# Kernel tuning notes

Measured on AMD Instinct MI355X. Metric: run time of the kernel, lower is better.

## Reference

```python
import jax, jax.numpy as jnp
import numpy as np

B, S, E = 2, 2048, 1024
H, D = 16, 64  # num_heads, head_size; H*D == E

def setup_inputs() -> dict:
    key = jax.random.key(0)
    k1, k2, k3 = jax.random.split(key, 3)
    x = jax.random.normal(k1, (B, S, E), dtype=jnp.float32)
    w_qkv = jax.random.normal(k2, (E, 3 * H * D), dtype=jnp.float32) / np.sqrt(E)
    b_qkv = jnp.zeros((3 * H * D,), dtype=jnp.float32)
    w_out = jax.random.normal(k3, (H * D, E), dtype=jnp.float32) / np.sqrt(H * D)
    b_out = jnp.zeros((E,), dtype=jnp.float32)
    return {"x": x, "w_qkv": w_qkv, "b_qkv": b_qkv, "w_out": w_out, "b_out": b_out}

def reference(x, w_qkv, b_qkv, w_out, b_out):
    b, s, e = x.shape
    qkv = x @ w_qkv + b_qkv                       # [b, s, 3*H*D]
    qkv = qkv.reshape(b, s, 3, H, D).transpose(2, 0, 3, 1, 4)  # [3, b, H, s, D]
    q, k, v = qkv[0], qkv[1], qkv[2]
    scores = jnp.einsum('bhqd,bhkd->bhqk', q, k) / jnp.sqrt(jnp.float32(D))
    mask = jnp.tril(jnp.ones((s, s), dtype=scores.dtype))
    scores = scores * mask - 1e10 * (1 - mask)
    attn = jax.nn.softmax(scores, axis=-1)
    out = jnp.einsum('bhqk,bhkd->bhqd', attn, v)  # [b, H, s, D]
    out = out.transpose(0, 2, 1, 3).reshape(b, s, H * D)
    return out @ w_out + b_out
```

## Files before the change

kernel.cpp:

```cpp
#include <hip/hip_runtime.h>

typedef unsigned short u16;
typedef __attribute__((ext_vector_type(8))) short bf16x8;
typedef __attribute__((ext_vector_type(4))) float f32x4;

#define S_LEN 2048
#define MTOT  4096
#define LOG2E_DIV8 0.1803368784f

__device__ inline u16 f2bf(float f) {
  union { float f; unsigned u; } x; x.f = f;
  unsigned r = x.u + 0x7fffu + ((x.u >> 16) & 1u);
  return (u16)(r >> 16);
}
__device__ inline float bf2f(u16 u) {
  union { unsigned u; float f; } x; x.u = ((unsigned)u) << 16;
  return x.f;
}

__device__ __forceinline__ unsigned cvtpk_bf16(float lo, float hi) {
  unsigned r;
  asm("v_cvt_pk_bf16_f32 %0, %1, %2" : "=v"(r) : "v"(lo), "v"(hi));
  return r;
}
__device__ __forceinline__ float fexp2(float x) {
  float r;
  asm("v_exp_f32 %0, %1" : "=v"(r) : "v"(x));
  return r;
}
__device__ __forceinline__ float frcp(float x) {
  float r;
  asm("v_rcp_f32 %0, %1" : "=v"(r) : "v"(x));
  return r;
}

#define SWAP32(a, b) asm("v_permlane32_swap_b32 %0, %1" : "+v"(a), "+v"(b))
#define SWAP16(a, b) asm("v_permlane16_swap_b32 %0, %1" : "+v"(a), "+v"(b))

__device__ __forceinline__ float sum_lg(float x) {
  float a = x, b = x;
  SWAP32(a, b);
  float s = a + b;
  float c = s, d = s;
  SWAP16(c, d);
  return c + d;
}

typedef __attribute__((address_space(1))) const unsigned int gu32;
typedef __attribute__((address_space(3))) unsigned int lu32;
__device__ __forceinline__ void gload_lds16(const void* g, void* l) {
  __builtin_amdgcn_global_load_lds((gu32*)g, (lu32*)l, 16, 0, 0);
}

#define MFMA16(a, b, c) __builtin_amdgcn_mfma_f32_16x16x32_bf16((a), (b), (c), 0, 0, 0)
#define BAR  __builtin_amdgcn_s_barrier()
#define VMC6 asm volatile("s_waitcnt vmcnt(6)" ::: "memory")
#define VMC0 asm volatile("s_waitcnt vmcnt(0)" ::: "memory")

__global__ __launch_bounds__(256) void prep(const float* __restrict__ x,
                                            const float* __restrict__ wqkv,
                                            const float* __restrict__ wout,
                                            u16* __restrict__ x_bf,
                                            u16* __restrict__ dqkv,
                                            u16* __restrict__ dwout) {
  __shared__ float tile[64][65];
  int bid = blockIdx.x;
  int t = threadIdx.x;
  if (bid < 4096) {
    int i = (bid * 256 + t) * 4;
    float4 v = *(const float4*)(x + i);
    ushort4 o;
    o.x = f2bf(v.x); o.y = f2bf(v.y); o.z = f2bf(v.z); o.w = f2bf(v.w);
    *(ushort4*)(x_bf + i) = o;
    return;
  }
  int idx = bid - 4096;
  int bx = idx & 63, by = idx >> 6;
  const float* src; u16* dst; int N, n0;
  if (bx < 48) { src = wqkv; dst = dqkv; N = 3072; n0 = bx * 64; }
  else         { src = wout; dst = dwout; N = 1024; n0 = (bx - 48) * 64; }
  int K = 1024, k0 = by * 64;
  for (int i = 0; i < 16; ++i) {
    int id2 = t + 256 * i;
    int r = id2 >> 6, c = id2 & 63;
    tile[r][c] = src[(size_t)(k0 + r) * N + n0 + c];
  }
  __syncthreads();
  for (int i = 0; i < 16; ++i) {
    int id2 = t + 256 * i;
    int r = id2 >> 6, c = id2 & 63;
    dst[(size_t)(n0 + r) * K + k0 + c] = f2bf(tile[c][r]);
  }
}

__global__ __launch_bounds__(512, 1) void gemm_qkv(const u16* __restrict__ A,
                                                   const u16* __restrict__ Bt,
                                                   const float* __restrict__ bias,
                                                   u16* __restrict__ qkv,
                                                   u16* __restrict__ Vt,
                                                   float qscale) {
  __shared__ __align__(16) u16 smem[65536];
  int t = threadIdx.x;
  int w = t >> 6, l = t & 63;
  int wr = w >> 2, wcn = w & 3;
  int lr = l & 15, lg = l >> 4;

  int bid = blockIdx.y * 12 + blockIdx.x;
  int orig = (bid & 7) * 24 + (bid >> 3);
  int bx = orig % 12, by = orig / 12;
  int m0 = by * 256, n0 = bx * 256;

  f32x4 acc[8][4];
#pragma unroll
  for (int i = 0; i < 8; ++i)
#pragma unroll
    for (int j = 0; j < 4; ++j)
      acc[i][j] = f32x4{0.f, 0.f, 0.f, 0.f};

  int cg = ((t & 7) ^ ((t >> 3) & 7)) * 8;
  const u16* gAh[2][2];
  const u16* gBh[2][2];
#pragma unroll
  for (int h = 0; h < 2; ++h)
#pragma unroll
    for (int j = 0; j < 2; ++j) {
      gAh[h][j] = A  + (size_t)(m0 + h * 128 + j * 64 + (t >> 3)) * 1024 + cg;
      gBh[h][j] = Bt + (size_t)(n0 + h * 128 + j * 64 + (t >> 3)) * 1024 + cg;
    }

#define STG_A(kt, h) {                                                  \
    u16* d_ = smem + (((kt) & 1) * 2 + (h)) * 8192 + t * 8;             \
    gload_lds16(gAh[h][0] + (size_t)(kt) * 64, d_);                     \
    gload_lds16(gAh[h][1] + (size_t)(kt) * 64, d_ + 4096);              }
#define STG_B(kt, h) {                                                  \
    u16* d_ = smem + 32768 + (((kt) & 1) * 2 + (h)) * 8192 + t * 8;     \
    gload_lds16(gBh[h][0] + (size_t)(kt) * 64, d_);                     \
    gload_lds16(gBh[h][1] + (size_t)(kt) * 64, d_ + 4096);              }

  int o0 = lr * 64 + ((lg ^ (lr & 7)) << 3);
  int o1 = lr * 64 + (((4 + lg) ^ (lr & 7)) << 3);
  const u16* bA[2] = { smem + wr * 8192, smem + (2 + wr) * 8192 };
  const u16* bB[2] = { smem + 32768 + (wcn >> 1) * 8192 + (wcn & 1) * 4096,
                       smem + 32768 + (2 + (wcn >> 1)) * 8192 + (wcn & 1) * 4096 };

  bf16x8 AF[4][2], Bf[4][2];
#define LDA(B_, OFF) { const u16* p_ = bA[B_] + (OFF);                  \
    _Pragma("unroll") for (int mi = 0; mi < 4; ++mi) {                  \
      AF[mi][0] = *(const bf16x8*)(p_ + mi * 1024 + o0);                \
      AF[mi][1] = *(const bf16x8*)(p_ + mi * 1024 + o1); } }
#define LDB(B_) { const u16* p_ = bB[B_];                               \
    _Pragma("unroll") for (int ni = 0; ni < 4; ++ni) {                  \
      Bf[ni][0] = *(const bf16x8*)(p_ + ni * 1024 + o0);                \
      Bf[ni][1] = *(const bf16x8*)(p_ + ni * 1024 + o1); } }
#define QUAD(MO, NO) {                                                  \
    __builtin_amdgcn_s_setprio(1);                                      \
    _Pragma("unroll") for (int mi = 0; mi < 4; ++mi)                    \
    _Pragma("unroll") for (int ni = 0; ni < 2; ++ni) {                  \
      acc[MO + mi][NO + ni] = MFMA16(AF[mi][0], Bf[NO + ni][0], acc[MO + mi][NO + ni]); \
      acc[MO + mi][NO + ni] = MFMA16(AF[mi][1], Bf[NO + ni][1], acc[MO + mi][NO + ni]); } \
    __builtin_amdgcn_s_setprio(0); }

  STG_B(0, 0); STG_B(0, 1); STG_A(0, 0); STG_A(0, 1);
  STG_B(1, 0); STG_B(1, 1); STG_A(1, 0);
  VMC6;
  BAR;

  for (int i = 0; i < 8; ++i) {
    bool s = (i < 7);
    int k0t = 2 * i, k1t = 2 * i + 1;
    LDA(0, 0); LDB(0);
    STG_A(k1t, 1);
    BAR; QUAD(0, 0); BAR;
    if (s) STG_B(k0t + 2, 0);
    BAR; QUAD(0, 2); BAR;
    LDA(0, 4096);
    if (s) STG_B(k0t + 2, 1);
    BAR; QUAD(4, 0); BAR;
    if (s) STG_A(k0t + 2, 0);
    if (i == 7) { VMC0; } else { VMC6; }
    BAR; QUAD(4, 2); BAR;
    LDA(1, 0); LDB(1);
    if (s) STG_A(k0t + 2, 1);
    BAR; QUAD(0, 0); BAR;
    if (s) STG_B(k1t + 2, 0);
    BAR; QUAD(0, 2); BAR;
    LDA(1, 4096);
    if (s) STG_B(k1t + 2, 1);
    BAR; QUAD(4, 0); BAR;
    if (s) STG_A(k1t + 2, 0);
    VMC6;
    BAR; QUAD(4, 2); BAR;
  }
#undef STG_A
#undef STG_B
#undef LDA
#undef LDB
#undef QUAD

  if (bx < 8) {
    float qs = (bx < 4) ? qscale : 1.0f;
#pragma unroll
    for (int mi = 0; mi < 8; ++mi)
#pragma unroll
      for (int ni = 0; ni < 4; ++ni)
#pragma unroll
        for (int rg = 0; rg < 4; ++rg) {
          int row = m0 + wr * 128 + mi * 16 + lg * 4 + rg;
          int col = n0 + wcn * 64 + ni * 16 + lr;
          qkv[(size_t)row * 3072 + col] = f2bf((acc[mi][ni][rg] + bias[col]) * qs);
        }
    return;
  }

  int b = by >> 3, sbase = (by & 7) * 256;
  u16* Vl = smem;
#pragma unroll 1
  for (int g = 0; g < 4; ++g) {
    __syncthreads();
    if (wcn == g) {
#pragma unroll
      for (int mi = 0; mi < 8; ++mi)
#pragma unroll
        for (int ni = 0; ni < 4; ++ni) {
          int d = ni * 16 + lr;
          int srow = wr * 128 + mi * 16 + lg * 4;
          int col = n0 + g * 64 + d;
          union { u16 u[4]; unsigned long long q; } pk;
#pragma unroll
          for (int rg = 0; rg < 4; ++rg)
            pk.u[rg] = f2bf(acc[mi][ni][rg] + bias[col]);
          *(unsigned long long*)&Vl[d * 272 + srow] = pk.q;
        }
    }
    __syncthreads();
    int hv = (bx - 8) * 4 + g;
    int d = t >> 3, sc = (t & 7) * 32;
    u16* dst = Vt + ((size_t)((b * 16 + hv) * 64 + d)) * 2048 + sbase + sc;
    const u16* src = Vl + d * 272 + sc;
#pragma unroll
    for (int j = 0; j < 4; ++j)
      *(uint4*)(dst + j * 8) = *(const uint4*)(src + j * 8);
  }
}

__global__ __launch_bounds__(256) void gemm_bt64(const u16* __restrict__ A,
                                                 const u16* __restrict__ Bt,
                                                 const float* __restrict__ bias,
                                                 float* __restrict__ C,
                                                 int N, int K) {
  __shared__ __align__(16) u16 smem[2][6144];
  int t = threadIdx.x;
  int w = t >> 6, l = t & 63;
  int lr = l & 15, lg = l >> 4;

  int nwg = gridDim.x * gridDim.y;
  int bid = blockIdx.y * gridDim.x + blockIdx.x;
  int orig = (bid & 7) * (nwg >> 3) + (bid >> 3);
  int bx = orig % gridDim.x, by = orig / gridDim.x;
  int m0 = by * 64, n0 = bx * 128;

  f32x4 acc[4][2];
#pragma unroll
  for (int i = 0; i < 4; ++i)
#pragma unroll
    for (int j = 0; j < 2; ++j)
      acc[i][j] = f32x4{0.f, 0.f, 0.f, 0.f};

  int ra = w * 16 + (l >> 2);
  int ca = (l & 3) ^ ((ra >> 1) & 3);
  int rb1 = ra + 64;
  int cb1 = (l & 3) ^ ((rb1 >> 1) & 3);
  const u16* gA  = A  + (size_t)(m0 + ra) * K + ca * 8;
  const u16* gB0 = Bt + (size_t)(n0 + ra) * K + ca * 8;
  const u16* gB1 = Bt + (size_t)(n0 + rb1) * K + cb1 * 8;
  int oA  = (w * 16) * 32;
  int oB0 = 2048 + (w * 16) * 32;
  int oB1 = 2048 + (64 + w * 16) * 32;

#define STAGE(K0, BUF) {                                   \
    gload_lds16(gA + (K0), &smem[BUF][oA]);                \
    gload_lds16(gB0 + (K0), &smem[BUF][oB0]);              \
    gload_lds16(gB1 + (K0), &smem[BUF][oB1]);              }

  STAGE(0, 0);
  __syncthreads();
  int cur = 0;
  for (int k0 = 0; k0 < K; k0 += 32) {
    if (k0 + 32 < K) STAGE(k0 + 32, cur ^ 1);
    const u16* As = smem[cur];
    const u16* Bs = smem[cur] + 2048;
    bf16x8 af[4], bfr[2];
#pragma unroll
    for (int mi = 0; mi < 4; ++mi) {
      int row = mi * 16 + lr;
      af[mi] = *(const bf16x8*)(As + row * 32 + ((lg ^ ((row >> 1) & 3)) << 3));
    }
#pragma unroll
    for (int ni = 0; ni < 2; ++ni) {
      int row = w * 32 + ni * 16 + lr;
      bfr[ni] = *(const bf16x8*)(Bs + row * 32 + ((lg ^ ((row >> 1) & 3)) << 3));
    }
    __builtin_amdgcn_s_setprio(1);
#pragma unroll
    for (int mi = 0; mi < 4; ++mi)
#pragma unroll
      for (int ni = 0; ni < 2; ++ni)
        acc[mi][ni] = MFMA16(af[mi], bfr[ni], acc[mi][ni]);
    __builtin_amdgcn_s_setprio(0);
    __syncthreads();
    cur ^= 1;
  }
#undef STAGE

#pragma unroll
  for (int mi = 0; mi < 4; ++mi)
#pragma unroll
    for (int ni = 0; ni < 2; ++ni)
#pragma unroll
      for (int rg = 0; rg < 4; ++rg) {
        int row = m0 + mi * 16 + lg * 4 + rg;
        int col = n0 + w * 32 + ni * 16 + lr;
        C[(size_t)row * N + col] = acc[mi][ni][rg] + bias[col];
      }
}

__device__ __forceinline__ void attn_tile(const u16* Ks, const u16* Vs,
                                          bf16x8 q0, bf16x8 q1, f32x4* o,
                                          float& l_run, bool diag,
                                          int w, int l, int lr, int lg) {
  f32x4 s[4];
  __builtin_amdgcn_s_setprio(1);
#pragma unroll
  for (int ct = 0; ct < 4; ++ct) {
    int row = ct * 16 + lr;
    bf16x8 kf0 = *(const bf16x8*)(Ks + ((row * 64 + lg * 8) ^ ((row & 7) << 3)));
    bf16x8 kf1 = *(const bf16x8*)(Ks + ((row * 64 + 32 + lg * 8) ^ ((row & 7) << 3)));
    f32x4 z = f32x4{0.f, 0.f, 0.f, 0.f};
    z = MFMA16(kf0, q0, z);
    z = MFMA16(kf1, q1, z);
    s[ct] = z;
  }
  __builtin_amdgcn_s_setprio(0);
  if (diag) {
    int qrel = w * 16 + lr;
#pragma unroll
    for (int ct = 0; ct < 4; ++ct)
#pragma unroll
      for (int rg = 0; rg < 4; ++rg)
        if ((ct * 16 + lg * 4 + rg) > qrel) s[ct][rg] = -1e30f;
  }
  float ps = 0.f;
#pragma unroll
  for (int ct = 0; ct < 4; ++ct)
#pragma unroll
    for (int rg = 0; rg < 4; ++rg) {
      float p = fexp2(s[ct][rg]);
      s[ct][rg] = p;
      ps += p;
    }
  l_run += sum_lg(ps);

  unsigned W00 = cvtpk_bf16(s[0][0], s[0][1]);
  unsigned W01 = cvtpk_bf16(s[0][2], s[0][3]);
  unsigned W10 = cvtpk_bf16(s[1][0], s[1][1]);
  unsigned W11 = cvtpk_bf16(s[1][2], s[1][3]);
  unsigned W20 = cvtpk_bf16(s[2][0], s[2][1]);
  unsigned W21 = cvtpk_bf16(s[2][2], s[2][3]);
  unsigned W30 = cvtpk_bf16(s[3][0], s[3][1]);
  unsigned W31 = cvtpk_bf16(s[3][2], s[3][3]);
  SWAP32(W00, W10); SWAP16(W00, W10);
  SWAP32(W01, W11); SWAP16(W01, W11);
  SWAP32(W20, W30); SWAP16(W20, W30);
  SWAP32(W21, W31); SWAP16(W21, W31);
  union { unsigned u[4]; bf16x8 v; } P0, P1;
  P0.u[0] = W00; P0.u[1] = W01; P0.u[2] = W10; P0.u[3] = W11;
  P1.u[0] = W20; P1.u[1] = W21; P1.u[2] = W30; P1.u[3] = W31;

  __builtin_amdgcn_s_setprio(1);
#pragma unroll
  for (int dt = 0; dt < 4; ++dt) {
    int row = dt * 16 + lr;
    bf16x8 vf0 = *(const bf16x8*)(Vs + ((row * 64 + lg * 8) ^ ((row & 7) << 3)));
    bf16x8 vf1 = *(const bf16x8*)(Vs + ((row * 64 + 32 + lg * 8) ^ ((row & 7) << 3)));
    o[dt] = MFMA16(P0.v, vf0, o[dt]);
    o[dt] = MFMA16(P1.v, vf1, o[dt]);
  }
  __builtin_amdgcn_s_setprio(0);
}

__global__ __launch_bounds__(256, 4) void attn_kernel(const u16* __restrict__ qkv,
                                                      const u16* __restrict__ Vt,
                                                      u16* __restrict__ po0,
                                                      u16* __restrict__ po1,
                                                      float* __restrict__ pl) {
  __shared__ __align__(16) u16 Ks[2][64 * 64];
  __shared__ __align__(16) u16 Vs[2][64 * 64];
  int bid = blockIdx.y * 32 + blockIdx.x;
  int orig = (bid & 7) * 128 + (bid >> 3);
  int half = orig & 1;
  int qtA = (orig >> 1) & 15;
  int bh = orig >> 5;
  int qtB = 31 - qtA;
  int m = (qtA >= 8) ? 8 : (15 - qtA);
  int kts = half ? m : 0;
  int kte = half ? (qtB + 1) : m;
  int b = bh >> 4, h = bh & 15;
  int t = threadIdx.x, w = t >> 6, l = t & 63;
  int lr = l & 15, lg = l >> 4;

  const u16* qbase = qkv + (size_t)b * S_LEN * 3072 + h * 64;
  int qrA = qtA * 64 + w * 16 + lr;
  int qrB = qtB * 64 + w * 16 + lr;
  bf16x8 qA0 = *(const bf16x8*)(qbase + (size_t)qrA * 3072 + lg * 8);
  bf16x8 qA1 = *(const bf16x8*)(qbase + (size_t)qrA * 3072 + 32 + lg * 8);
  bf16x8 qB0 = *(const bf16x8*)(qbase + (size_t)qrB * 3072 + lg * 8);
  bf16x8 qB1 = *(const bf16x8*)(qbase + (size_t)qrB * 3072 + 32 + lg * 8);

  f32x4 oA[4], oB[4];
#pragma unroll
  for (int i = 0; i < 4; ++i) { oA[i] = f32x4{0.f,0.f,0.f,0.f}; oB[i] = f32x4{0.f,0.f,0.f,0.f}; }
  float lA = 0.f, lB = 0.f;

  int r0s = t >> 3, r1s = r0s + 32;
  int soff = (t & 7) * 8;
  int e0 = (r0s * 64 + soff) ^ ((r0s & 7) << 3);
  int e1 = (r1s * 64 + soff) ^ ((r1s & 7) << 3);
  const u16* Kg = qkv + (size_t)b * S_LEN * 3072 + 1024 + h * 64 + soff;
  const u16* Vg = Vt + (size_t)bh * 64 * S_LEN + soff;

  uint4 k0r, k1r, v0r, v1r;
#define ISSUE(KT) {                                                     \
    int kk0 = (KT) * 64;                                                \
    k0r = *(const uint4*)(Kg + (size_t)(kk0 + r0s) * 3072);             \
    k1r = *(const uint4*)(Kg + (size_t)(kk0 + r1s) * 3072);             \
    v0r = *(const uint4*)(Vg + (size_t)r0s * S_LEN + kk0);              \
    v1r = *(const uint4*)(Vg + (size_t)r1s * S_LEN + kk0);              }

  ISSUE(kts);
  *(uint4*)(Ks[0] + e0) = k0r;
  *(uint4*)(Ks[0] + e1) = k1r;
  *(uint4*)(Vs[0] + e0) = v0r;
  *(uint4*)(Vs[0] + e1) = v1r;
  if (kts + 1 < kte) ISSUE(kts + 1);
  __syncthreads();

  int cur = 0;
  for (int kt = kts; kt < kte; ++kt) {
    if (kt + 1 < kte) {
      u16* Kd = Ks[cur ^ 1];
      u16* Vd = Vs[cur ^ 1];
      *(uint4*)(Kd + e0) = k0r;
      *(uint4*)(Kd + e1) = k1r;
      *(uint4*)(Vd + e0) = v0r;
      *(uint4*)(Vd + e1) = v1r;
    }
    if (kt + 2 < kte) ISSUE(kt + 2);
    const u16* Kc = Ks[cur];
    const u16* Vc = Vs[cur];
    if (kt <= qtA)
      attn_tile(Kc, Vc, qA0, qA1, oA, lA, kt == qtA, w, l, lr, lg);
    attn_tile(Kc, Vc, qB0, qB1, oB, lB, kt == qtB, w, l, lr, lg);
    __syncthreads();
    cur ^= 1;
  }
#undef ISSUE

  u16* po = half ? po1 : po0;
  float* plh = pl + half * 65536;
#pragma unroll
  for (int dt = 0; dt < 4; ++dt)
#pragma unroll
    for (int rg = 0; rg < 4; ++rg) {
      int d = dt * 16 + lr;
      int qA_ = qtA * 64 + w * 16 + lg * 4 + rg;
      int qB_ = qtB * 64 + w * 16 + lg * 4 + rg;
      po[(size_t)(b * S_LEN + qA_) * 1024 + h * 64 + d] = f2bf(oA[dt][rg]);
      po[(size_t)(b * S_LEN + qB_) * 1024 + h * 64 + d] = f2bf(oB[dt][rg]);
    }
  if (lg == 0) {
    plh[bh * 2048 + qtA * 64 + w * 16 + lr] = lA;
    plh[bh * 2048 + qtB * 64 + w * 16 + lr] = lB;
  }
}

__global__ __launch_bounds__(256) void attn_combine(const u16* po0,
                                                    const u16* __restrict__ po1,
                                                    const float* __restrict__ pl,
                                                    u16* out) {
  int i = (blockIdx.x * 256 + threadIdx.x) * 8;
  int row = i >> 10;
  int h = (i & 1023) >> 6;
  int bh = (row >> 11) * 16 + h;
  int q = row & 2047;
  float r = frcp(pl[bh * 2048 + q] + pl[65536 + bh * 2048 + q]);
  bf16x8 a = *(const bf16x8*)(po0 + i);
  bf16x8 c = *(const bf16x8*)(po1 + i);
  union { u16 u[8]; bf16x8 v; } o;
#pragma unroll
  for (int j = 0; j < 8; ++j)
    o.u[j] = f2bf((bf2f((u16)a[j]) + bf2f((u16)c[j])) * r);
  *(bf16x8*)(out + i) = o.v;
}

extern "C" void kernel_launch(void* const* d_in, const int* in_sizes, int n_in,
                              void* d_out, int out_size, void* d_ws, size_t ws_size,
                              hipStream_t stream) {
  const float* x     = (const float*)d_in[0];
  const float* w_qkv = (const float*)d_in[1];
  const float* b_qkv = (const float*)d_in[2];
  const float* w_out = (const float*)d_in[3];
  const float* b_out = (const float*)d_in[4];
  float* out = (float*)d_out;

  char* ws = (char*)d_ws;
  u16* x_bf   = (u16*)(ws);
  u16* po1    = (u16*)(ws);
  u16* wqkvT  = (u16*)(ws + ( 8ull << 20));
  float* pl   = (float*)(ws + ( 8ull << 20));
  u16* woutT  = (u16*)(ws + (14ull << 20));
  u16* qkv    = (u16*)(ws + (16ull << 20));
  u16* Vt     = (u16*)(ws + (40ull << 20));
  u16* po0    = (u16*)(ws + (48ull << 20));
  u16* attnb  = (u16*)(ws + (48ull << 20));

  prep<<<4096 + 1024, 256, 0, stream>>>(x, w_qkv, w_out, x_bf, wqkvT, woutT);
  gemm_qkv<<<dim3(12, 16), 512, 0, stream>>>(x_bf, wqkvT, b_qkv, qkv, Vt,
                                             LOG2E_DIV8);
  attn_kernel<<<dim3(32, 32), 256, 0, stream>>>(qkv, Vt, po0, po1, pl);
  attn_combine<<<MTOT * 1024 / (256 * 8), 256, 0, stream>>>(po0, po1, pl, attnb);
  gemm_bt64<<<dim3(8, 64), 256, 0, stream>>>(attnb, woutT, b_out, out, 1024, 1024);
}
```

Measured before the change: 108.0 us.

## Retile QKV GEMM to 256x192 tiles so the grid fills all CUs

```diff
diff --git a/kernel.cpp b/kernel.cpp
--- a/kernel.cpp
+++ b/kernel.cpp
@@ -54,7 +54,7 @@
 
 #define MFMA16(a, b, c) __builtin_amdgcn_mfma_f32_16x16x32_bf16((a), (b), (c), 0, 0, 0)
 #define BAR  __builtin_amdgcn_s_barrier()
-#define VMC6 asm volatile("s_waitcnt vmcnt(6)" ::: "memory")
+#define VMC5 asm volatile("s_waitcnt vmcnt(5)" ::: "memory")
 #define VMC0 asm volatile("s_waitcnt vmcnt(0)" ::: "memory")
 
 __global__ __launch_bounds__(256) void prep(const float* __restrict__ x,
@@ -99,70 +99,76 @@
                                                    u16* __restrict__ qkv,
                                                    u16* __restrict__ Vt,
                                                    float qscale) {
-  __shared__ __align__(16) u16 smem[65536];
+  __shared__ __align__(16) u16 smem[57344];
   int t = threadIdx.x;
   int w = t >> 6, l = t & 63;
   int wr = w >> 2, wcn = w & 3;
   int lr = l & 15, lg = l >> 4;
 
-  int bid = blockIdx.y * 12 + blockIdx.x;
-  int orig = (bid & 7) * 24 + (bid >> 3);
-  int bx = orig % 12, by = orig / 12;
-  int m0 = by * 256, n0 = bx * 256;
-
-  f32x4 acc[8][4];
+  int bid = blockIdx.y * 16 + blockIdx.x;
+  int orig = (bid & 7) * 32 + (bid >> 3);
+  int bx = orig & 15, by = orig >> 4;
+  int m0 = by * 256, n0 = bx * 192;
+
+  f32x4 acc[8][3];
 #pragma unroll
   for (int i = 0; i < 8; ++i)
 #pragma unroll
-    for (int j = 0; j < 4; ++j)
+    for (int j = 0; j < 3; ++j)
       acc[i][j] = f32x4{0.f, 0.f, 0.f, 0.f};
 
   int cg = ((t & 7) ^ ((t >> 3) & 7)) * 8;
   const u16* gAh[2][2];
-  const u16* gBh[2][2];
+  const u16* gB3[3];
 #pragma unroll
   for (int h = 0; h < 2; ++h)
 #pragma unroll
-    for (int j = 0; j < 2; ++j) {
-      gAh[h][j] = A  + (size_t)(m0 + h * 128 + j * 64 + (t >> 3)) * 1024 + cg;
-      gBh[h][j] = Bt + (size_t)(n0 + h * 128 + j * 64 + (t >> 3)) * 1024 + cg;
-    }
+    for (int j = 0; j < 2; ++j)
+      gAh[h][j] = A + (size_t)(m0 + h * 128 + j * 64 + (t >> 3)) * 1024 + cg;
+#pragma unroll
+  for (int th = 0; th < 3; ++th)
+    gB3[th] = Bt + (size_t)(n0 + th * 64 + (t >> 3)) * 1024 + cg;
 
 #define STG_A(kt, h) {                                                  \
     u16* d_ = smem + (((kt) & 1) * 2 + (h)) * 8192 + t * 8;             \
     gload_lds16(gAh[h][0] + (size_t)(kt) * 64, d_);                     \
     gload_lds16(gAh[h][1] + (size_t)(kt) * 64, d_ + 4096);              }
-#define STG_B(kt, h) {                                                  \
-    u16* d_ = smem + 32768 + (((kt) & 1) * 2 + (h)) * 8192 + t * 8;     \
-    gload_lds16(gBh[h][0] + (size_t)(kt) * 64, d_);                     \
-    gload_lds16(gBh[h][1] + (size_t)(kt) * 64, d_ + 4096);              }
-
-  int o0 = lr * 64 + ((lg ^ (lr & 7)) << 3);
-  int o1 = lr * 64 + (((4 + lg) ^ (lr & 7)) << 3);
+#define STG_B3(kt, th) {                                                \
+    u16* d_ = smem + 32768 + (((kt) & 1) * 3 + (th)) * 4096 + t * 8;    \
+    gload_lds16(gB3[th] + (size_t)(kt) * 64, d_);                       }
+
+  int co0 = (lg ^ (lr & 7)) << 3;
+  int co1 = ((4 + lg) ^ (lr & 7)) << 3;
   const u16* bA[2] = { smem + wr * 8192, smem + (2 + wr) * 8192 };
-  const u16* bB[2] = { smem + 32768 + (wcn >> 1) * 8192 + (wcn & 1) * 4096,
-                       smem + 32768 + (2 + (wcn >> 1)) * 8192 + (wcn & 1) * 4096 };
-
-  bf16x8 AF[4][2], Bf[4][2];
-#define LDA(B_, OFF) { const u16* p_ = bA[B_] + (OFF);                  \
+  const u16* bB[2] = { smem + 32768, smem + 32768 + 12288 };
+  int rB = (48 * wcn + lr) * 64;
+
+  bf16x8 AF[4][2], Bf[3][2];
+#define LDA(B_, OFF) { const u16* p_ = bA[B_] + (OFF) + lr * 64;        \
     _Pragma("unroll") for (int mi = 0; mi < 4; ++mi) {                  \
-      AF[mi][0] = *(const bf16x8*)(p_ + mi * 1024 + o0);                \
-      AF[mi][1] = *(const bf16x8*)(p_ + mi * 1024 + o1); } }
-#define LDB(B_) { const u16* p_ = bB[B_];                               \
-    _Pragma("unroll") for (int ni = 0; ni < 4; ++ni) {                  \
-      Bf[ni][0] = *(const bf16x8*)(p_ + ni * 1024 + o0);                \
-      Bf[ni][1] = *(const bf16x8*)(p_ + ni * 1024 + o1); } }
-#define QUAD(MO, NO) {                                                  \
+      AF[mi][0] = *(const bf16x8*)(p_ + mi * 1024 + co0);               \
+      AF[mi][1] = *(const bf16x8*)(p_ + mi * 1024 + co1); } }
+#define LDB(B_) { const u16* p_ = bB[B_] + rB;                          \
+    _Pragma("unroll") for (int ni = 0; ni < 3; ++ni) {                  \
+      Bf[ni][0] = *(const bf16x8*)(p_ + ni * 1024 + co0);               \
+      Bf[ni][1] = *(const bf16x8*)(p_ + ni * 1024 + co1); } }
+#define QUADa(MO) {                                                     \
     __builtin_amdgcn_s_setprio(1);                                      \
     _Pragma("unroll") for (int mi = 0; mi < 4; ++mi)                    \
     _Pragma("unroll") for (int ni = 0; ni < 2; ++ni) {                  \
-      acc[MO + mi][NO + ni] = MFMA16(AF[mi][0], Bf[NO + ni][0], acc[MO + mi][NO + ni]); \
-      acc[MO + mi][NO + ni] = MFMA16(AF[mi][1], Bf[NO + ni][1], acc[MO + mi][NO + ni]); } \
+      acc[MO + mi][ni] = MFMA16(AF[mi][0], Bf[ni][0], acc[MO + mi][ni]); \
+      acc[MO + mi][ni] = MFMA16(AF[mi][1], Bf[ni][1], acc[MO + mi][ni]); } \
     __builtin_amdgcn_s_setprio(0); }
-
-  STG_B(0, 0); STG_B(0, 1); STG_A(0, 0); STG_A(0, 1);
-  STG_B(1, 0); STG_B(1, 1); STG_A(1, 0);
-  VMC6;
+#define QUADb(MO) {                                                     \
+    __builtin_amdgcn_s_setprio(1);                                      \
+    _Pragma("unroll") for (int mi = 0; mi < 4; ++mi) {                  \
+      acc[MO + mi][2] = MFMA16(AF[mi][0], Bf[2][0], acc[MO + mi][2]);   \
+      acc[MO + mi][2] = MFMA16(AF[mi][1], Bf[2][1], acc[MO + mi][2]); } \
+    __builtin_amdgcn_s_setprio(0); }
+
+  STG_B3(0, 0); STG_B3(0, 1); STG_B3(0, 2); STG_A(0, 0); STG_A(0, 1);
+  STG_B3(1, 0); STG_B3(1, 1); STG_B3(1, 2); STG_A(1, 0);
+  VMC5;
   BAR;
 
   for (int i = 0; i < 8; ++i) {
@@ -170,70 +176,76 @@
     int k0t = 2 * i, k1t = 2 * i + 1;
     LDA(0, 0); LDB(0);
     STG_A(k1t, 1);
-    BAR; QUAD(0, 0); BAR;
-    if (s) STG_B(k0t + 2, 0);
-    BAR; QUAD(0, 2); BAR;
+    BAR; QUADa(0); BAR;
+    if (s) { STG_B3(k0t + 2, 0); STG_B3(k0t + 2, 1); }
+    BAR; QUADb(0); BAR;
     LDA(0, 4096);
-    if (s) STG_B(k0t + 2, 1);
-    BAR; QUAD(4, 0); BAR;
+    if (s) STG_B3(k0t + 2, 2);
+    BAR; QUADa(4); BAR;
     if (s) STG_A(k0t + 2, 0);
-    if (i == 7) { VMC0; } else { VMC6; }
-    BAR; QUAD(4, 2); BAR;
+    if (i == 7) { VMC0; } else { VMC5; }
+    BAR; QUADb(4); BAR;
     LDA(1, 0); LDB(1);
     if (s) STG_A(k0t + 2, 1);
-    BAR; QUAD(0, 0); BAR;
-    if (s) STG_B(k1t + 2, 0);
-    BAR; QUAD(0, 2); BAR;
+    BAR; QUADa(0); BAR;
+    if (s) { STG_B3(k1t + 2, 0); STG_B3(k1t + 2, 1); }
+    BAR; QUADb(0); BAR;
     LDA(1, 4096);
-    if (s) STG_B(k1t + 2, 1);
-    BAR; QUAD(4, 0); BAR;
+    if (s) STG_B3(k1t + 2, 2);
+    BAR; QUADa(4); BAR;
     if (s) STG_A(k1t + 2, 0);
-    VMC6;
-    BAR; QUAD(4, 2); BAR;
+    VMC5;
+    BAR; QUADb(4); BAR;
   }
 #undef STG_A
-#undef STG_B
+#undef STG_B3
 #undef LDA
 #undef LDB
-#undef QUAD
-
-  if (bx < 8) {
-    float qs = (bx < 4) ? qscale : 1.0f;
-#pragma unroll
-    for (int mi = 0; mi < 8; ++mi)
-#pragma unroll
-      for (int ni = 0; ni < 4; ++ni)
+#undef QUADa
+#undef QUADb
+
+#pragma unroll
+  for (int ni = 0; ni < 3; ++ni) {
+    int cb = n0 + wcn * 48 + ni * 16;
+    if (cb < 2048) {
+      float qs = (cb < 1024) ? qscale : 1.0f;
+#pragma unroll
+      for (int mi = 0; mi < 8; ++mi)
 #pragma unroll
         for (int rg = 0; rg < 4; ++rg) {
           int row = m0 + wr * 128 + mi * 16 + lg * 4 + rg;
-          int col = n0 + wcn * 64 + ni * 16 + lr;
+          int col = cb + lr;
           qkv[(size_t)row * 3072 + col] = f2bf((acc[mi][ni][rg] + bias[col]) * qs);
         }
-    return;
-  }
-
+    }
+  }
+  int gvs = 32 - 3 * bx;
+  if (gvs < 0) gvs = 0;
   int b = by >> 3, sbase = (by & 7) * 256;
   u16* Vl = smem;
-#pragma unroll 1
-  for (int g = 0; g < 4; ++g) {
+#pragma unroll
+  for (int g = 0; g < 3; ++g) {
+    if (g < gvs) continue;
     __syncthreads();
-    if (wcn == g) {
-#pragma unroll
-      for (int mi = 0; mi < 8; ++mi)
-#pragma unroll
-        for (int ni = 0; ni < 4; ++ni) {
-          int d = ni * 16 + lr;
+#pragma unroll
+    for (int ni = 0; ni < 3; ++ni) {
+      int blk = 3 * wcn + ni;
+      if (blk >= 4 * g && blk < 4 * g + 4) {
+        int d = (blk - 4 * g) * 16 + lr;
+        int col = n0 + blk * 16 + lr;
+#pragma unroll
+        for (int mi = 0; mi < 8; ++mi) {
           int srow = wr * 128 + mi * 16 + lg * 4;
-          int col = n0 + g * 64 + d;
           union { u16 u[4]; unsigned long long q; } pk;
 #pragma unroll
           for (int rg = 0; rg < 4; ++rg)
             pk.u[rg] = f2bf(acc[mi][ni][rg] + bias[col]);
           *(unsigned long long*)&Vl[d * 272 + srow] = pk.q;
         }
+      }
     }
     __syncthreads();
-    int hv = (bx - 8) * 4 + g;
+    int hv = 3 * bx + g - 32;
     int d = t >> 3, sc = (t & 7) * 32;
     u16* dst = Vt + ((size_t)((b * 16 + hv) * 64 + d)) * 2048 + sbase + sc;
     const u16* src = Vl + d * 272 + sc;
@@ -524,7 +536,7 @@
   u16* attnb  = (u16*)(ws + (48ull << 20));
 
   prep<<<4096 + 1024, 256, 0, stream>>>(x, w_qkv, w_out, x_bf, wqkvT, woutT);
-  gemm_qkv<<<dim3(12, 16), 512, 0, stream>>>(x_bf, wqkvT, b_qkv, qkv, Vt,
+  gemm_qkv<<<dim3(16, 16), 512, 0, stream>>>(x_bf, wqkvT, b_qkv, qkv, Vt,
                                              LOG2E_DIV8);
   attn_kernel<<<dim3(32, 32), 256, 0, stream>>>(qkv, Vt, po0, po1, pl);
   attn_combine<<<MTOT * 1024 / (256 * 8), 256, 0, stream>>>(po0, po1, pl, attnb);
```

Result: faster. 101.7 us (-5.9%).
